# Performance work log

Hardware: AMD Instinct MI355X
Metric: run time of the kernel (lower is better)

The kernel has to match this reference:

```python
import jax, jax.numpy as jnp
import numpy as np
import math

N_HEADS = 12
HEAD_SIZE = 64
D_MODEL = 768
N_BASIS = 256
LENGTH = 1024
BATCH = 8
INV_SQRT_2PI = 1.0 / math.sqrt(2.0 * math.pi)


def _phi(t):
    # standard normal pdf
    return INV_SQRT_2PI * jnp.exp(-0.5 * t * t)


def _make_basis():
    # get_gaussian_basis_functions: meshgrid(linspace(0,1,N/2), sigmas).flatten()
    sigmas = np.array([0.01, 0.05], dtype=np.float32)
    mus = np.linspace(0.0, 1.0, N_BASIS // 2, dtype=np.float32)
    mu_b = np.repeat(mus, 2)          # [N]
    sigma_b = np.tile(sigmas, N_BASIS // 2)  # [N]
    return jnp.asarray(mu_b), jnp.asarray(sigma_b)


def _make_G(mu_b, sigma_b, klen, ridge=1.0):
    # compute_G: positions (i+1)/l, F[j,i] = psi_j(pos_i), G = F^T (F F^T + I)^{-1}
    pos = jnp.arange(1, klen + 1, dtype=jnp.float32) / klen
    F = _phi((pos[None, :] - mu_b[:, None]) / sigma_b[:, None]) / sigma_b[:, None]  # [N, klen]
    A = F @ F.T + ridge * jnp.eye(N_BASIS, dtype=jnp.float32)
    return F.T @ jnp.linalg.inv(A)  # [klen, N]


def setup_inputs() -> dict:
    key = jax.random.key(0)
    ks = jax.random.split(key, 8)
    sc = 1.0 / math.sqrt(D_MODEL)
    x = jax.random.normal(ks[0], (LENGTH, BATCH, D_MODEL), jnp.float32)
    q = jax.random.normal(ks[1], (LENGTH, BATCH, D_MODEL), jnp.float32)
    Wq = jax.random.normal(ks[2], (D_MODEL, D_MODEL), jnp.float32) * sc
    Wk = jax.random.normal(ks[3], (D_MODEL, D_MODEL), jnp.float32) * sc
    Wv = jax.random.normal(ks[4], (D_MODEL, D_MODEL), jnp.float32) * sc
    Wo = jax.random.normal(ks[5], (D_MODEL, D_MODEL), jnp.float32) * sc
    w_mu = jax.random.normal(ks[6], (N_BASIS,), jnp.float32) * (1.0 / math.sqrt(N_BASIS))
    w_sigma = jax.random.normal(ks[7], (N_BASIS,), jnp.float32) * (1.0 / math.sqrt(N_BASIS))
    mu_b, sigma_b = _make_basis()
    G = _make_G(mu_b, sigma_b, LENGTH)
    return {"x": x, "q": q, "Wq": Wq, "Wk": Wk, "Wv": Wv, "Wo": Wo,
            "w_mu": w_mu, "w_sigma": w_sigma, "mu_b": mu_b, "sigma_b": sigma_b, "G": G}


def reference(x, q, Wq, Wk, Wv, Wo, w_mu, w_sigma, mu_b, sigma_b, G):
    klen, B, d = x.shape
    qlen = q.shape[0]
    H, dh = N_HEADS, HEAD_SIZE
    # value_function: compress memory onto basis coefficients, B_mat: [B, N, d]
    Bmat = jnp.einsum('lbd,ln->bnd', x, G)
    keys = (Bmat @ Wk.T).reshape(B, N_BASIS, H, dh).transpose(0, 2, 1, 3)    # [B,H,N,dh]
    values = (Bmat @ Wv.T).reshape(B, N_BASIS, H, dh).transpose(0, 2, 1, 3)  # [B,H,N,dh]
    query = (q.transpose(1, 0, 2) @ Wq.T).reshape(B, qlen, H, dh).transpose(0, 2, 1, 3)
    scores = jnp.einsum('bhqe,bhne->bhqn', query, keys) / math.sqrt(dh)      # [B,H,q,N]
    # attention distribution parameters (theta -> (mu, sigma_sq) exactly)
    mu = jax.nn.sigmoid(scores @ w_mu)          # [B,H,q]
    sigma_sq = jax.nn.softplus(scores @ w_sigma)  # [B,H,q]
    # ContinuousSoftmax forward: E_{N(mu,sigma_sq)}[psi_j]
    #   = N(mu; mu_b_j, sigma_b_j^2 + sigma_sq)   (product-of-Gaussians integral)
    s = jnp.sqrt(sigma_b[None, None, None, :] ** 2 + sigma_sq[..., None])
    r = _phi((mu[..., None] - mu_b[None, None, None, :]) / s) / s            # [B,H,q,N]
    context = jnp.einsum('bhqn,bhnd->bhqd', r, values)                       # [B,H,q,dh]
    context = context.transpose(0, 2, 1, 3).reshape(B, qlen, H * dh)
    return context @ Wo.T  # [B, qlen, d_model]
```

## Files before the change

### kernel.cpp

```cpp
#include <hip/hip_runtime.h>
#include <hip/hip_bf16.h>
#include <math.h>

#define NHEADS 12
#define HEAD   64
#define DM     768
#define NB     256
#define SLEN   1024
#define NBATCH 8

typedef __bf16 bf16x8 __attribute__((ext_vector_type(8)));
typedef float  f32x4  __attribute__((ext_vector_type(4)));

__device__ __forceinline__ float gload(const void* p, long i, int bf) {
  return bf ? __bfloat162float(((const __hip_bfloat16*)p)[i])
            : ((const float*)p)[i];
}

__global__ void detect_dtype(const void* x, int* flag) {
  __shared__ float red[256];
  int t = threadIdx.x;
  const __hip_bfloat16* p = (const __hip_bfloat16*)x;
  float a = fabsf(__bfloat162float(p[t * 2]));
  float b = fabsf(__bfloat162float(p[t * 2 + 1]));
  float m = fmaxf(a, b);
  red[t] = m;
  __syncthreads();
  for (int s = 128; s > 0; s >>= 1) {
    if (t < s) red[t] = fmaxf(red[t], red[t + s]);
    __syncthreads();
  }
  if (t == 0) flag[0] = (red[0] < 1e4f) ? 1 : 0;
}

__global__ __launch_bounds__(256) void prep(
    const void* __restrict__ Wq, const void* __restrict__ Wk,
    const void* __restrict__ wmu, const void* __restrict__ wsig,
    const void* __restrict__ mub, const void* __restrict__ sigb,
    const void* __restrict__ G, const void* __restrict__ x,
    const void* __restrict__ Wv, const void* __restrict__ Wo,
    float* __restrict__ Wqf, float* __restrict__ Wkf,
    float* __restrict__ wmuf, float* __restrict__ wsigf,
    float* __restrict__ mubf, float* __restrict__ sigbf,
    __hip_bfloat16* __restrict__ Gth, __hip_bfloat16* __restrict__ Gtl,
    __hip_bfloat16* __restrict__ XCh, __hip_bfloat16* __restrict__ XCl,
    __hip_bfloat16* __restrict__ Wvh, __hip_bfloat16* __restrict__ Wvl,
    __hip_bfloat16* __restrict__ Woh, __hip_bfloat16* __restrict__ Wol,
    const int* __restrict__ flagp) {
  __shared__ float tl[64][65];
  const int blk = blockIdx.x, tid = threadIdx.x;
  const int bf = flagp[0];

  if (blk < 1152) {
    const void* src = (blk < 576) ? Wq : Wk;
    float* dst = (blk < 576) ? Wqf : Wkf;
    int rb = (blk < 576) ? blk : blk - 576;
    int i0 = (rb * 256 + tid) * 4;
#pragma unroll
    for (int j = 0; j < 4; j++) dst[i0 + j] = gload(src, i0 + j, bf);
  } else if (blk < 1156) {
    int which = blk - 1152;
    const void* src = (which == 0) ? wmu : (which == 1) ? wsig
                      : (which == 2) ? mub : sigb;
    float* dst = (which == 0) ? wmuf : (which == 1) ? wsigf
                 : (which == 2) ? mubf : sigbf;
    dst[tid] = gload(src, tid, bf);
  } else if (blk < 2756) {
    const void* src;
    __hip_bfloat16 *dh, *dl;
    int R = 1024, C, bx, by;
    if (blk < 1220) {
      int sub = blk - 1156;
      src = G; dh = Gth; dl = Gtl; C = 256; bx = sub % 4; by = sub / 4;
    } else {
      int sub = blk - 1220;
      src = x; dh = XCh; dl = XCl; C = 6144; bx = sub % 96; by = sub / 96;
    }
    int r0 = by * 64, c0 = bx * 64;
    int cl = tid & 63, rl = tid >> 6;
#pragma unroll
    for (int i = 0; i < 16; i++) {
      int rr = rl + i * 4;
      tl[rr][cl] = gload(src, (long)(r0 + rr) * C + c0 + cl, bf);
    }
    __syncthreads();
#pragma unroll
    for (int i = 0; i < 16; i++) {
      int cc = rl + i * 4;
      float f = tl[cl][cc];
      __hip_bfloat16 h = __float2bfloat16(f);
      long o = (long)(c0 + cc) * R + r0 + cl;
      dh[o] = h;
      dl[o] = __float2bfloat16(f - __bfloat162float(h));
    }
  } else {
    const void* src = (blk < 3332) ? Wv : Wo;
    __hip_bfloat16* dh = (blk < 3332) ? Wvh : Woh;
    __hip_bfloat16* dl = (blk < 3332) ? Wvl : Wol;
    int rb = (blk < 3332) ? blk - 2756 : blk - 3332;
    int i0 = (rb * 256 + tid) * 4;
#pragma unroll
    for (int j = 0; j < 4; j++) {
      float f = gload(src, i0 + j, bf);
      __hip_bfloat16 h = __float2bfloat16(f);
      dh[i0 + j] = h;
      dl[i0 + j] = __float2bfloat16(f - __bfloat162float(h));
    }
  }
}

__device__ __forceinline__ void stage_tile(
    const __hip_bfloat16* __restrict__ src, int ld, __hip_bfloat16* lds, int t) {
  int row = t >> 2;
  int col = (t & 3) * 8;
  int wavebase = (t >> 6) * 1024;
#pragma unroll
  for (int i = 0; i < 2; i++) {
    const __hip_bfloat16* gp = src + (long)(i * 64 + row) * ld + col;
    __builtin_amdgcn_global_load_lds(
        (const __attribute__((address_space(1))) void*)gp,
        (__attribute__((address_space(3))) void*)((char*)lds + i * 4096 + wavebase),
        16, 0, 0);
  }
}

__global__ __launch_bounds__(256) void mfma_nt_lds(
    const __hip_bfloat16* __restrict__ Ah_g, const __hip_bfloat16* __restrict__ Al_g,
    const __hip_bfloat16* __restrict__ Wh_g, const __hip_bfloat16* __restrict__ Wl_g,
    void* __restrict__ Cout, int K, int lda, int ldb, long a_batch, long c_batch,
    int om, int oh, const int* __restrict__ flagp, int use_flag, int pmask_bf,
    int ksplit, long kslab) {
  int flag = flagp[0];
  int bf = use_flag ? flag : 0;
  __shared__ __hip_bfloat16 As0[4096], As1[4096];
  __shared__ __hip_bfloat16 Bs0[4096], Bs1[4096];

  const int gx = gridDim.x, gy = gridDim.y;
  const int nwg = gx * gy * gridDim.z;
  const int lin = (blockIdx.z * gy + blockIdx.y) * gx + blockIdx.x;
  const int swz = (lin & 7) * (nwg >> 3) + (lin >> 3);
  const int bx = swz % gx;
  const int rem = swz / gx;
  const int by = rem % gy;
  const int bzf = rem / gy;
  const int bz = bzf / ksplit;
  const int kc = bzf - bz * ksplit;
  const int Ks = K / ksplit;
  const int kbeg = kc * Ks, kend = kbeg + Ks;

  const int m0 = by * 128, n0 = bx * 128;
  const int t = threadIdx.x;
  const int lane = t & 63;
  const int r = lane & 15, g = lane >> 4;
  const int wave = t >> 6;
  const int wm = (wave >> 1) * 64, wn = (wave & 1) * 64;

  const __hip_bfloat16* Abh = Ah_g + (long)bz * a_batch;
  const __hip_bfloat16* Abl = Al_g + (long)bz * a_batch;

  f32x4 zero4 = {0.f, 0.f, 0.f, 0.f};
  f32x4 acc[4][4];
#pragma unroll
  for (int fi = 0; fi < 4; fi++)
#pragma unroll
    for (int fj = 0; fj < 4; fj++) acc[fi][fj] = zero4;

  for (int pass = 0; pass < 3; pass++) {
    if (flag && !((pmask_bf >> pass) & 1)) continue;
    const __hip_bfloat16* Arow = ((pass < 2) ? Abh : Abl) + (long)m0 * lda;
    const __hip_bfloat16* Brow = ((pass == 1) ? Wl_g : Wh_g) + (long)n0 * ldb;
    stage_tile(Arow + kbeg, lda, As0, t);
    stage_tile(Brow + kbeg, ldb, Bs0, t);
    __syncthreads();
    int cur = 0;
    for (int k0 = kbeg; k0 < kend; k0 += 32) {
      const __hip_bfloat16* Asc = cur ? As1 : As0;
      const __hip_bfloat16* Bsc = cur ? Bs1 : Bs0;
      bf16x8 af[4], bw[4];
#pragma unroll
      for (int fi = 0; fi < 4; fi++)
        af[fi] = *(const bf16x8*)(Asc + (wm + fi * 16 + r) * 32 + g * 8);
#pragma unroll
      for (int fj = 0; fj < 4; fj++)
        bw[fj] = *(const bf16x8*)(Bsc + (wn + fj * 16 + r) * 32 + g * 8);
      if (k0 + 32 < kend) {
        stage_tile(Arow + k0 + 32, lda, cur ? As0 : As1, t);
        stage_tile(Brow + k0 + 32, ldb, cur ? Bs0 : Bs1, t);
      }
#pragma unroll
      for (int fi = 0; fi < 4; fi++)
#pragma unroll
        for (int fj = 0; fj < 4; fj++)
          acc[fi][fj] = __builtin_amdgcn_mfma_f32_16x16x32_bf16(
              af[fi], bw[fj], acc[fi][fj], 0, 0, 0);
      __syncthreads();
      cur ^= 1;
    }
  }

  if (ksplit > 1) {
    float* Cf = (float*)Cout + (long)kc * kslab;
#pragma unroll
    for (int fi = 0; fi < 4; fi++)
#pragma unroll
      for (int fj = 0; fj < 4; fj++)
#pragma unroll
        for (int v = 0; v < 4; v++) {
          int m = m0 + wm + fi * 16 + g * 4 + v;
          int n = n0 + wn + fj * 16 + r;
          long off = (long)bz * c_batch + (long)m * om + (long)(n >> 6) * oh + (n & 63);
          Cf[off] = acc[fi][fj][v];
        }
  } else {
#pragma unroll
    for (int fi = 0; fi < 4; fi++)
#pragma unroll
      for (int fj = 0; fj < 4; fj++)
#pragma unroll
        for (int v = 0; v < 4; v++) {
          int m = m0 + wm + fi * 16 + g * 4 + v;
          int n = n0 + wn + fj * 16 + r;
          long off = (long)bz * c_batch + (long)m * om + (long)(n >> 6) * oh + (n & 63);
          float val = acc[fi][fj][v];
          if (bf) ((__hip_bfloat16*)Cout)[off] = __float2bfloat16(val);
          else    ((float*)Cout)[off] = val;
        }
  }
}

__global__ __launch_bounds__(256) void reduce_split(
    const float* __restrict__ slabs, float* __restrict__ outf,
    __hip_bfloat16* __restrict__ dh, __hip_bfloat16* __restrict__ dl) {
  long i0 = ((long)blockIdx.x * 256 + threadIdx.x) * 4;
  f32x4 s = *(const f32x4*)(slabs + i0);
#pragma unroll
  for (int k = 1; k < 4; k++) {
    f32x4 v = *(const f32x4*)(slabs + (long)k * 1572864 + i0);
    s.x += v.x; s.y += v.y; s.z += v.z; s.w += v.w;
  }
  *(f32x4*)(outf + i0) = s;
#pragma unroll
  for (int j = 0; j < 4; j++) {
    float f = s[j];
    __hip_bfloat16 h = __float2bfloat16(f);
    dh[i0 + j] = h;
    dl[i0 + j] = __float2bfloat16(f - __bfloat162float(h));
  }
}

__global__ __launch_bounds__(256) void vtsplit_sum(
    const float* __restrict__ slabs, __hip_bfloat16* __restrict__ dh,
    __hip_bfloat16* __restrict__ dl) {
  __shared__ float tle[64][65];
  const int z = blockIdx.y;
  const int r0 = blockIdx.x * 64;
  int cl = threadIdx.x & 63, rl4 = threadIdx.x >> 6;
#pragma unroll
  for (int i = 0; i < 16; i++) {
    int rr = rl4 + i * 4;
    long idx = (long)z * 16384 + (r0 + rr) * 64 + cl;
    float s = slabs[idx];
#pragma unroll
    for (int k = 1; k < 4; k++) s += slabs[(long)k * 1572864 + idx];
    tle[rr][cl] = s;
  }
  __syncthreads();
#pragma unroll
  for (int i = 0; i < 16; i++) {
    int cc = rl4 + i * 4;
    float f = tle[cl][cc];
    __hip_bfloat16 h = __float2bfloat16(f);
    long o = (long)z * 16384 + (long)cc * 256 + r0 + cl;
    dh[o] = h;
    dl[o] = __float2bfloat16(f - __bfloat162float(h));
  }
}

__global__ __launch_bounds__(256) void bvec(
    const float* __restrict__ Bmat, const float* __restrict__ wmuf,
    const float* __restrict__ wsigf, float* __restrict__ bmu,
    float* __restrict__ bsig) {
  int t = blockIdx.x * 256 + threadIdx.x;
  int w = t / 6144, r = t % 6144;
  const float* wv = w ? wsigf : wmuf;
  float acc = 0.f;
  for (int n = 0; n < NB; n++) acc += wv[n] * Bmat[(long)n * 6144 + r];
  (w ? bsig : bmu)[r] = acc;
}

__global__ __launch_bounds__(256) void kvec(
    const float* __restrict__ Wkf, const float* __restrict__ bmu,
    const float* __restrict__ bsig, float* __restrict__ kmu,
    float* __restrict__ ksig) {
  int t = blockIdx.x * 256 + threadIdx.x;
  int w = t / 6144, r = t % 6144;
  int b = r / 768, c = r % 768;
  const float* bv = (w ? bsig : bmu) + b * 768;
  const float* wk = Wkf + (long)c * 768;
  float acc = 0.f;
  for (int d = 0; d < 768; d++) acc += bv[d] * wk[d];
  (w ? ksig : kmu)[r] = acc;
}

__global__ __launch_bounds__(256) void wqvec(
    const float* __restrict__ Wqf, const float* __restrict__ kmu,
    const float* __restrict__ ksig, float* __restrict__ wqm,
    float* __restrict__ wqs) {
  int t = blockIdx.x * 256 + threadIdx.x;
  int w = t / 73728, r = t % 73728;
  int b = r / 9216, h = (r % 9216) / 768, d = r % 768;
  const float* kv = (w ? ksig : kmu) + b * 768 + h * 64;
  float acc = 0.f;
  for (int dh = 0; dh < 64; dh++)
    acc += Wqf[(long)(h * 64 + dh) * 768 + d] * kv[dh];
  (w ? wqs : wqm)[r] = acc;
}

__global__ __launch_bounds__(256) void amu_kernel(
    const void* __restrict__ q, const float* __restrict__ wqm,
    const float* __restrict__ wqs, float* __restrict__ amu,
    const int* __restrict__ flagp) {
  int bf = flagp[0];
  int lane = threadIdx.x & 63;
  int wave = threadIdx.x >> 6;
  int qrow = blockIdx.x * 4 + wave;
  int b = blockIdx.y;
  float qv[12];
  long base = ((long)qrow * 8 + b) * 768 + lane;
#pragma unroll
  for (int j = 0; j < 12; j++) qv[j] = gload(q, base + 64 * j, bf);
  for (int hh = 0; hh < 24; hh++) {
    const float* vec = (hh < 12) ? (wqm + ((long)b * 12 + hh) * 768)
                                 : (wqs + ((long)b * 12 + hh - 12) * 768);
    float p = 0.f;
#pragma unroll
    for (int j = 0; j < 12; j++) p += qv[j] * vec[lane + 64 * j];
#pragma unroll
    for (int m = 32; m >= 1; m >>= 1) p += __shfl_xor(p, m);
    if (lane == 0) amu[((long)b * 24 + hh) * 1024 + qrow] = p;
  }
}

__global__ __launch_bounds__(256) void attn_mfma(
    const __hip_bfloat16* __restrict__ Vth, const __hip_bfloat16* __restrict__ Vtl,
    const float* __restrict__ amu, const float* __restrict__ mubf,
    const float* __restrict__ sigbf, __hip_bfloat16* __restrict__ Ch,
    __hip_bfloat16* __restrict__ Cl) {
  const int qch = blockIdx.x, h = blockIdx.y, b = blockIdx.z;
  const int t = threadIdx.x;
  const int lane = t & 63, wave = t >> 6;
  const int r = lane & 15, g = lane >> 4;
  const int wq = wave * 32;
  __shared__ float s_mub[NB], s_sb2[NB];
  {
    float sb = sigbf[t];
    s_mub[t] = mubf[t];
    s_sb2[t] = sb * sb;
  }
  __syncthreads();

  float mu_[2], sig_[2];
#pragma unroll
  for (int fi = 0; fi < 2; fi++) {
    int q = qch * 128 + wq + fi * 16 + r;
    float araw = amu[((long)b * 24 + h) * 1024 + q] * 0.125f;
    float sraw = amu[((long)b * 24 + 12 + h) * 1024 + q] * 0.125f;
    mu_[fi] = 1.f / (1.f + expf(-araw));
    sig_[fi] = fmaxf(sraw, 0.f) + log1pf(expf(-fabsf(sraw)));
  }

  const __hip_bfloat16* vhb = Vth + ((long)b * 12 + h) * 16384;
  const __hip_bfloat16* vlb = Vtl + ((long)b * 12 + h) * 16384;

  f32x4 zero4 = {0.f, 0.f, 0.f, 0.f};
  f32x4 acc[2][4];
#pragma unroll
  for (int fi = 0; fi < 2; fi++)
#pragma unroll
    for (int fj = 0; fj < 4; fj++) acc[fi][fj] = zero4;

  for (int ks = 0; ks < 8; ks++) {
    bf16x8 rh[2], rl[2];
#pragma unroll
    for (int fi = 0; fi < 2; fi++) {
      float mu = mu_[fi], sg = sig_[fi];
#pragma unroll
      for (int j = 0; j < 8; j++) {
        int n = ks * 32 + g * 8 + j;
        float inv_s = rsqrtf(s_sb2[n] + sg);
        float tt = (mu - s_mub[n]) * inv_s;
        float rv = 0.3989422804014327f * inv_s *
                   exp2f(-0.7213475204444817f * tt * tt);
        __bf16 hi = (__bf16)rv;
        rh[fi][j] = hi;
        rl[fi][j] = (__bf16)(rv - (float)hi);
      }
    }
#pragma unroll
    for (int fj = 0; fj < 4; fj++) {
      long vo = (long)(fj * 16 + r) * 256 + ks * 32 + g * 8;
      bf16x8 vh = *(const bf16x8*)(vhb + vo);
      bf16x8 vl = *(const bf16x8*)(vlb + vo);
#pragma unroll
      for (int fi = 0; fi < 2; fi++) {
        acc[fi][fj] = __builtin_amdgcn_mfma_f32_16x16x32_bf16(
            rh[fi], vh, acc[fi][fj], 0, 0, 0);
        acc[fi][fj] = __builtin_amdgcn_mfma_f32_16x16x32_bf16(
            rl[fi], vh, acc[fi][fj], 0, 0, 0);
        acc[fi][fj] = __builtin_amdgcn_mfma_f32_16x16x32_bf16(
            rh[fi], vl, acc[fi][fj], 0, 0, 0);
      }
    }
  }

#pragma unroll
  for (int fi = 0; fi < 2; fi++)
#pragma unroll
    for (int fj = 0; fj < 4; fj++)
#pragma unroll
      for (int v = 0; v < 4; v++) {
        int q = qch * 128 + wq + fi * 16 + g * 4 + v;
        int d = fj * 16 + r;
        long off = ((long)(b * SLEN + q)) * DM + h * HEAD + d;
        float f = acc[fi][fj][v];
        __hip_bfloat16 hh = __float2bfloat16(f);
        Ch[off] = hh;
        Cl[off] = __float2bfloat16(f - __bfloat162float(hh));
      }
}

extern "C" void kernel_launch(void* const* d_in, const int* in_sizes, int n_in,
                              void* d_out, int out_size, void* d_ws, size_t ws_size,
                              hipStream_t stream) {
  const void* x    = d_in[0];
  const void* q    = d_in[1];
  const void* Wq   = d_in[2];
  const void* Wk   = d_in[3];
  const void* Wv   = d_in[4];
  const void* Wo   = d_in[5];
  const void* wmu  = d_in[6];
  const void* wsig = d_in[7];
  const void* mub  = d_in[8];
  const void* sigb = d_in[9];
  const void* G    = d_in[10];

  int* flagp = (int*)d_ws;
  float* base = (float*)d_ws + 16;
  float* Wqf   = base;
  float* Wkf   = Wqf + 589824;
  float* wmuf  = Wkf + 589824;
  float* wsigf = wmuf + 256;
  float* mubf  = wsigf + 256;
  float* sigbf = mubf + 256;
  float* Bmat  = sigbf + 256;
  float* slab1 = Bmat + 1572864;
  float* wqm   = slab1 + 6291456;
  float* wqs   = wqm + 73728;
  float* amu   = wqs + 73728;
  float* bmu   = amu + 196608;
  float* bsig  = bmu + 6144;
  float* kmu   = bsig + 6144;
  float* ksig  = kmu + 6144;
  __hip_bfloat16* Wvh = (__hip_bfloat16*)(ksig + 6144);
  __hip_bfloat16* Wvl = Wvh + 589824;
  __hip_bfloat16* Woh = Wvl + 589824;
  __hip_bfloat16* Wol = Woh + 589824;
  __hip_bfloat16* Gth = Wol + 589824;
  __hip_bfloat16* Gtl = Gth + 262144;
  __hip_bfloat16* Bh  = Gtl + 262144;
  __hip_bfloat16* Bl  = Bh + 1572864;
  __hip_bfloat16* XCh = Bl + 1572864;
  __hip_bfloat16* XCl = XCh + 6291456;
  float* slab2 = (float*)XCh;
  __hip_bfloat16* Vth = XCl + 6291456;
  __hip_bfloat16* Vtl = Vth + 1572864;

  detect_dtype<<<1, 256, 0, stream>>>(x, flagp);

  prep<<<3908, 256, 0, stream>>>(
      Wq, Wk, wmu, wsig, mub, sigb, G, x, Wv, Wo,
      Wqf, Wkf, wmuf, wsigf, mubf, sigbf,
      Gth, Gtl, XCh, XCl, Wvh, Wvl, Woh, Wol, flagp);

  mfma_nt_lds<<<dim3(48, 2, 4), 256, 0, stream>>>(
      Gth, Gtl, XCh, XCl, slab1, 1024, 1024, 1024,
      0, 0, 6144, 64, flagp, 0,
      1, 4, 1572864);

  reduce_split<<<1536, 256, 0, stream>>>(slab1, Bmat, Bh, Bl);

  mfma_nt_lds<<<dim3(6, 2, 32), 256, 0, stream>>>(
      Bh, Bl, Wvh, Wvl, slab2, 768, 6144, 768,
      768, 196608, 64, 16384, flagp, 0,
      5, 4, 1572864);

  vtsplit_sum<<<dim3(4, 96), 256, 0, stream>>>(slab2, Vth, Vtl);

  bvec<<<48, 256, 0, stream>>>(Bmat, wmuf, wsigf, bmu, bsig);
  kvec<<<48, 256, 0, stream>>>(Wkf, bmu, bsig, kmu, ksig);
  wqvec<<<576, 256, 0, stream>>>(Wqf, kmu, ksig, wqm, wqs);
  amu_kernel<<<dim3(256, 8), 256, 0, stream>>>(q, wqm, wqs, amu, flagp);

  attn_mfma<<<dim3(8, 12, 8), 256, 0, stream>>>(
      Vth, Vtl, amu, mubf, sigbf, XCh, XCl);

  mfma_nt_lds<<<dim3(6, 64, 1), 256, 0, stream>>>(
      XCh, XCl, Woh, Wol, d_out, 768, 768, 768,
      0, 0, 768, 64, flagp, 1,
      5, 1, 0);
}
```

Measured before the change: 345.3 us.

## Fuse split-bf16 GEMM passes into shared rounds with 512 threads and swizzled LDS

Restructures the three-pass hi/lo split-bf16 GEMM into one or two rounds. Each round stages a third operand tile alongside A and W, so the hi operand is loaded once and reused for two MFMA products. The block grows to 512 threads (8 waves of 64x32 sub-tiles), and the LDS layout gets an XOR swizzle to cut bank conflicts on fragment reads. This aims to cut redundant global-to-LDS traffic and loop overhead, at the cost of more LDS per block and possibly lower occupancy.

```diff
diff --git a/kernel.cpp b/kernel.cpp
--- a/kernel.cpp
+++ b/kernel.cpp
@@ -109,22 +109,24 @@
   }
 }
 
-__device__ __forceinline__ void stage_tile(
+__device__ __forceinline__ void stage512(
     const __hip_bfloat16* __restrict__ src, int ld, __hip_bfloat16* lds, int t) {
   int row = t >> 2;
-  int col = (t & 3) * 8;
-  int wavebase = (t >> 6) * 1024;
-#pragma unroll
-  for (int i = 0; i < 2; i++) {
-    const __hip_bfloat16* gp = src + (long)(i * 64 + row) * ld + col;
-    __builtin_amdgcn_global_load_lds(
-        (const __attribute__((address_space(1))) void*)gp,
-        (__attribute__((address_space(3))) void*)((char*)lds + i * 4096 + wavebase),
-        16, 0, 0);
-  }
-}
-
-__global__ __launch_bounds__(256) void mfma_nt_lds(
+  int col = ((t & 3) ^ ((t >> 3) & 3)) * 8;
+  const __hip_bfloat16* gp = src + (long)row * ld + col;
+  __builtin_amdgcn_global_load_lds(
+      (const __attribute__((address_space(1))) void*)gp,
+      (__attribute__((address_space(3))) void*)((char*)lds + (t >> 6) * 1024),
+      16, 0, 0);
+}
+
+__device__ __forceinline__ bf16x8 frag_read(
+    const __hip_bfloat16* slot, int row, int g) {
+  int sl = g ^ ((row >> 1) & 3);
+  return *(const bf16x8*)(slot + row * 32 + sl * 8);
+}
+
+__global__ __launch_bounds__(512) void mfma_nt_lds(
     const __hip_bfloat16* __restrict__ Ah_g, const __hip_bfloat16* __restrict__ Al_g,
     const __hip_bfloat16* __restrict__ Wh_g, const __hip_bfloat16* __restrict__ Wl_g,
     void* __restrict__ Cout, int K, int lda, int ldb, long a_batch, long c_batch,
@@ -132,8 +134,7 @@
     int ksplit, long kslab) {
   int flag = flagp[0];
   int bf = use_flag ? flag : 0;
-  __shared__ __hip_bfloat16 As0[4096], As1[4096];
-  __shared__ __hip_bfloat16 Bs0[4096], Bs1[4096];
+  __shared__ __hip_bfloat16 S[2][3][4096];
 
   const int gx = gridDim.x, gy = gridDim.y;
   const int nwg = gx * gy * gridDim.z;
@@ -153,46 +154,86 @@
   const int lane = t & 63;
   const int r = lane & 15, g = lane >> 4;
   const int wave = t >> 6;
-  const int wm = (wave >> 1) * 64, wn = (wave & 1) * 64;
-
-  const __hip_bfloat16* Abh = Ah_g + (long)bz * a_batch;
-  const __hip_bfloat16* Abl = Al_g + (long)bz * a_batch;
+  const int wm = (wave >> 2) * 64, wn = (wave & 3) * 32;
+
+  const __hip_bfloat16* AhR = Ah_g + (long)bz * a_batch + (long)m0 * lda;
+  const __hip_bfloat16* AlR = Al_g + (long)bz * a_batch + (long)m0 * lda;
+  const __hip_bfloat16* WhR = Wh_g + (long)n0 * ldb;
+  const __hip_bfloat16* WlR = Wl_g + (long)n0 * ldb;
 
   f32x4 zero4 = {0.f, 0.f, 0.f, 0.f};
-  f32x4 acc[4][4];
+  f32x4 acc[4][2];
 #pragma unroll
   for (int fi = 0; fi < 4; fi++)
 #pragma unroll
-    for (int fj = 0; fj < 4; fj++) acc[fi][fj] = zero4;
-
-  for (int pass = 0; pass < 3; pass++) {
-    if (flag && !((pmask_bf >> pass) & 1)) continue;
-    const __hip_bfloat16* Arow = ((pass < 2) ? Abh : Abl) + (long)m0 * lda;
-    const __hip_bfloat16* Brow = ((pass == 1) ? Wl_g : Wh_g) + (long)n0 * ldb;
-    stage_tile(Arow + kbeg, lda, As0, t);
-    stage_tile(Brow + kbeg, ldb, Bs0, t);
+    for (int fj = 0; fj < 2; fj++) acc[fi][fj] = zero4;
+
+  int nrounds;
+  const __hip_bfloat16 *rA[2], *rW[2], *rX[2];
+  int rmode[2], rxld[2];
+  if (flag) {
+    nrounds = 1;
+    rA[0] = AhR; rW[0] = WhR; rX[0] = AlR;
+    rmode[0] = (pmask_bf & 4) ? 1 : 0; rxld[0] = lda;
+  } else {
+    nrounds = 2;
+    rA[0] = AhR; rW[0] = WhR; rX[0] = WlR; rmode[0] = 2; rxld[0] = ldb;
+    rA[1] = AlR; rW[1] = WhR; rX[1] = WhR; rmode[1] = 0; rxld[1] = ldb;
+  }
+
+  for (int rd = 0; rd < nrounds; rd++) {
+    const __hip_bfloat16* A0 = rA[rd];
+    const __hip_bfloat16* W0 = rW[rd];
+    const __hip_bfloat16* X0 = rX[rd];
+    const int md = rmode[rd], xld = rxld[rd];
+    stage512(A0 + kbeg, lda, S[0][0], t);
+    stage512(W0 + kbeg, ldb, S[0][1], t);
+    if (md) stage512(X0 + kbeg, xld, S[0][2], t);
     __syncthreads();
     int cur = 0;
     for (int k0 = kbeg; k0 < kend; k0 += 32) {
-      const __hip_bfloat16* Asc = cur ? As1 : As0;
-      const __hip_bfloat16* Bsc = cur ? Bs1 : Bs0;
-      bf16x8 af[4], bw[4];
+      bf16x8 af[4], bw[2], xf[4];
 #pragma unroll
       for (int fi = 0; fi < 4; fi++)
-        af[fi] = *(const bf16x8*)(Asc + (wm + fi * 16 + r) * 32 + g * 8);
-#pragma unroll
-      for (int fj = 0; fj < 4; fj++)
-        bw[fj] = *(const bf16x8*)(Bsc + (wn + fj * 16 + r) * 32 + g * 8);
+        af[fi] = frag_read(S[cur][0], wm + fi * 16 + r, g);
+#pragma unroll
+      for (int fj = 0; fj < 2; fj++)
+        bw[fj] = frag_read(S[cur][1], wn + fj * 16 + r, g);
+      if (md == 1) {
+#pragma unroll
+        for (int fi = 0; fi < 4; fi++)
+          xf[fi] = frag_read(S[cur][2], wm + fi * 16 + r, g);
+      } else if (md == 2) {
+#pragma unroll
+        for (int fj = 0; fj < 2; fj++)
+          xf[fj] = frag_read(S[cur][2], wn + fj * 16 + r, g);
+      }
       if (k0 + 32 < kend) {
-        stage_tile(Arow + k0 + 32, lda, cur ? As0 : As1, t);
-        stage_tile(Brow + k0 + 32, ldb, cur ? Bs0 : Bs1, t);
+        stage512(A0 + k0 + 32, lda, S[cur ^ 1][0], t);
+        stage512(W0 + k0 + 32, ldb, S[cur ^ 1][1], t);
+        if (md) stage512(X0 + k0 + 32, xld, S[cur ^ 1][2], t);
       }
 #pragma unroll
       for (int fi = 0; fi < 4; fi++)
 #pragma unroll
-        for (int fj = 0; fj < 4; fj++)
+        for (int fj = 0; fj < 2; fj++)
           acc[fi][fj] = __builtin_amdgcn_mfma_f32_16x16x32_bf16(
               af[fi], bw[fj], acc[fi][fj], 0, 0, 0);
+      if (md == 1) {
+#pragma unroll
+        for (int fi = 0; fi < 4; fi++)
+#pragma unroll
+          for (int fj = 0; fj < 2; fj++)
+            acc[fi][fj] = __builtin_amdgcn_mfma_f32_16x16x32_bf16(
+                xf[fi], bw[fj], acc[fi][fj], 0, 0, 0);
+      } else if (md == 2) {
+#pragma unroll
+        for (int fi = 0; fi < 4; fi++)
+#pragma unroll
+          for (int fj = 0; fj < 2; fj++)
+            acc[fi][fj] = __builtin_amdgcn_mfma_f32_16x16x32_bf16(
+                af[fi], xf[fj], acc[fi][fj], 0, 0, 0);
+      }
       __syncthreads();
       cur ^= 1;
     }
@@ -203,7 +244,7 @@
 #pragma unroll
     for (int fi = 0; fi < 4; fi++)
 #pragma unroll
-      for (int fj = 0; fj < 4; fj++)
+      for (int fj = 0; fj < 2; fj++)
 #pragma unroll
         for (int v = 0; v < 4; v++) {
           int m = m0 + wm + fi * 16 + g * 4 + v;
@@ -215,7 +256,7 @@
 #pragma unroll
     for (int fi = 0; fi < 4; fi++)
 #pragma unroll
-      for (int fj = 0; fj < 4; fj++)
+      for (int fj = 0; fj < 2; fj++)
 #pragma unroll
         for (int v = 0; v < 4; v++) {
           int m = m0 + wm + fi * 16 + g * 4 + v;
@@ -482,14 +523,14 @@
       Wqf, Wkf, wmuf, wsigf, mubf, sigbf,
       Gth, Gtl, XCh, XCl, Wvh, Wvl, Woh, Wol, flagp);
 
-  mfma_nt_lds<<<dim3(48, 2, 4), 256, 0, stream>>>(
+  mfma_nt_lds<<<dim3(48, 2, 4), 512, 0, stream>>>(
       Gth, Gtl, XCh, XCl, slab1, 1024, 1024, 1024,
       0, 0, 6144, 64, flagp, 0,
       1, 4, 1572864);
 
   reduce_split<<<1536, 256, 0, stream>>>(slab1, Bmat, Bh, Bl);
 
-  mfma_nt_lds<<<dim3(6, 2, 32), 256, 0, stream>>>(
+  mfma_nt_lds<<<dim3(6, 2, 32), 512, 0, stream>>>(
       Bh, Bl, Wvh, Wvl, slab2, 768, 6144, 768,
       768, 196608, 64, 16384, flagp, 0,
       5, 4, 1572864);
@@ -504,7 +545,7 @@
   attn_mfma<<<dim3(8, 12, 8), 256, 0, stream>>>(
       Vth, Vtl, amu, mubf, sigbf, XCh, XCl);
 
-  mfma_nt_lds<<<dim3(6, 64, 1), 256, 0, stream>>>(
+  mfma_nt_lds<<<dim3(6, 64, 1), 512, 0, stream>>>(
       XCh, XCl, Woh, Wol, d_out, 768, 768, 768,
       0, 0, 768, 64, flagp, 1,
       5, 1, 0);
```

Result: slower. 363.7 us (+5.3%).
